# Kernel tuning notes

Hardware: AMD Instinct MI355X
Metric: run time of the kernel (lower is better)

Reference implementation:

```python
import jax, jax.numpy as jnp
import numpy as np

N_NODES = 100000
N_EDGES = 1000000
NODE_DIM = 128
EDGE_DIM = 64
IN_DIM = 2 * NODE_DIM + EDGE_DIM  # 320


def _linear_init(key, fan_in, fan_out):
    # mimic torch nn.Linear default: U(-1/sqrt(fan_in), 1/sqrt(fan_in))
    kw, kb = jax.random.split(key)
    bound = 1.0 / np.sqrt(fan_in)
    W = jax.random.uniform(kw, (fan_in, fan_out), jnp.float32, -bound, bound)
    b = jax.random.uniform(kb, (fan_out,), jnp.float32, -bound, bound)
    return W, b


def setup_inputs() -> dict:
    key = jax.random.key(0)
    ks = jax.random.split(key, 8)
    x = jax.random.normal(ks[0], (N_NODES, NODE_DIM), jnp.float32)
    edge_index = jax.random.randint(ks[1], (2, N_EDGES), 0, N_NODES, jnp.int64 if jax.config.read('jax_enable_x64') else jnp.int32)
    edge_features = jax.random.normal(ks[2], (N_EDGES, EDGE_DIM), jnp.float32)
    W1, b1 = _linear_init(ks[3], IN_DIM, 256)
    W2, b2 = _linear_init(ks[4], 256, 128)
    W3, b3 = _linear_init(ks[5], 128, 64)
    W4, b4 = _linear_init(ks[6], 64, 1)
    return {
        'x': x, 'edge_index': edge_index, 'edge_features': edge_features,
        'num_nodes': N_NODES,
        'W1': W1, 'b1': b1, 'W2': W2, 'b2': b2,
        'W3': W3, 'b3': b3, 'W4': W4, 'b4': b4,
    }


def reference(x, edge_index, edge_features, num_nodes, W1, b1, W2, b2, W3, b3, W4, b4):
    v = edge_index[0]
    u = edge_index[1]
    # gather endpoint embeddings and concat with edge features: [E, 2*node_dim+edge_dim]
    pair = jnp.concatenate([x[v], x[u], edge_features], axis=-1)
    h = jax.nn.relu(pair @ W1 + b1)
    h = jax.nn.relu(h @ W2 + b2)
    h = jax.nn.relu(h @ W3 + b3)
    pred = h @ W4 + b4  # [E, 1]
    return pred
```

## Files before the change

kernel.cpp:

```cpp
#include <hip/hip_runtime.h>
#include <hip/hip_bf16.h>

typedef __bf16 bf16;
typedef __attribute__((ext_vector_type(8))) __bf16 bf16x8;
typedef __attribute__((ext_vector_type(4))) __bf16 bf16x4;
typedef __attribute__((ext_vector_type(4))) float f32x4;

#define E_TOTAL   1000000
#define NODE_DIM  128
#define EDGE_DIM  64

#define SA_STRIDE  328
#define SH1_STRIDE 264
#define SH2_STRIDE 136

#define SMEM_BYTES 51200
#define SH2_OFF    33792

#define WS_XBF_BYTES 25600000
#define WB_W2F  163840
#define WB_W3F  (163840 + 65536)
#define WB_CANO (163840 + 65536 + 16384)
#define WB_FLAG (163840 + 65536 + 16384 + 2064)
#define WB_END  (163840 + 65536 + 16384 + 2064 + 16)
#define WS_NEED (WS_XBF_BYTES + WB_END)

__device__ inline int plausible16(const unsigned short* h) {
    int c = 0;
    for (int i = 0; i < 64; ++i) {
        int e = (h[i] >> 7) & 0xFF;
        if (e >= 90 && e <= 151) ++c;
    }
    return c;
}

__global__ void sniff(const void* x, const void* ei, const void* ef,
                      const void* W1, int* flags) {
    if (threadIdx.x == 0 && blockIdx.x == 0) {
        flags[0] = (plausible16((const unsigned short*)x)  < 52) ? 1 : 0;
        flags[1] = (plausible16((const unsigned short*)ef) < 52) ? 1 : 0;
        flags[2] = (plausible16((const unsigned short*)W1) < 52) ? 1 : 0;
        const int* w = (const int*)ei;
        int oz = 0, lo_ok = 1;
        for (int i = 1; i < 32; i += 2) if (w[i] == 0) ++oz;
        for (int i = 0; i < 32; i += 2) if ((unsigned)w[i] >= 100000u) lo_ok = 0;
        flags[3] = (oz == 16 && lo_ok) ? 1 : 0;
    }
}

__device__ inline float loadF(const void* p, int isf, int i) {
    return isf ? ((const float*)p)[i] : (float)((const bf16*)p)[i];
}

__global__ void canonicalize(const void* W1, const void* W2, const void* W3,
                             const void* b1, const void* b2, const void* b3,
                             const void* W4, const void* b4,
                             bf16* W1f, bf16* W2f, bf16* W3f,
                             float* cano, const int* flags) {
    int isf = flags[2];
    int o = blockIdx.x * 256 + threadIdx.x;
    if (o < 81920) {
        int jj = o & 7, lane = (o >> 3) & 63, t2 = o >> 9;
        int ks = t2 % 10, jt = t2 / 10;
        int k = ks * 32 + (lane >> 4) * 8 + jj;
        int n = jt * 16 + (lane & 15);
        W1f[o] = (bf16)loadF(W1, isf, k * 256 + n);
    } else if (o < 114688) {
        int o2 = o - 81920;
        int jj = o2 & 7, lane = (o2 >> 3) & 63, t2 = o2 >> 9;
        int ks = t2 & 7, jt = t2 >> 3;
        int k = ks * 32 + (lane >> 4) * 8 + jj;
        int n = jt * 16 + (lane & 15);
        W2f[o2] = (bf16)loadF(W2, isf, k * 128 + n);
    } else if (o < 122880) {
        int o3 = o - 114688;
        int jj = o3 & 7, lane = (o3 >> 3) & 63, t2 = o3 >> 9;
        int ks = t2 & 3, jt = t2 >> 2;
        int k = ks * 32 + (lane >> 4) * 8 + jj;
        int n = jt * 16 + (lane & 15);
        W3f[o3] = (bf16)loadF(W3, isf, k * 64 + n);
    } else if (o < 123396) {
        int j = o - 122880;
        float v;
        if (j < 256)       v = loadF(b1, isf, j);
        else if (j < 384)  v = loadF(b2, isf, j - 256);
        else if (j < 448)  v = loadF(b3, isf, j - 384);
        else if (j == 448) v = loadF(b4, isf, 0);
        else if (j < 452)  v = 0.f;
        else               v = loadF(W4, isf, j - 452);
        cano[j] = v;
    }
}

__global__ void convert_x(const void* x, bf16* xbf, const int* flags) {
    int i = (blockIdx.x * 256 + threadIdx.x) * 4;
    if (flags[0]) {
        const float* f = (const float*)x + i;
        bf16 v0 = (bf16)f[0], v1 = (bf16)f[1], v2 = (bf16)f[2], v3 = (bf16)f[3];
        xbf[i] = v0; xbf[i + 1] = v1; xbf[i + 2] = v2; xbf[i + 3] = v3;
    } else {
        *(unsigned long long*)(xbf + i) = *(const unsigned long long*)((const bf16*)x + i);
    }
}

__global__ __launch_bounds__(256, 3) void fused_mlp(
    const void* __restrict__ xs, const int* __restrict__ ei, const void* __restrict__ ef,
    const bf16* __restrict__ W1f, const bf16* __restrict__ W2f,
    const bf16* __restrict__ W3f,
    const float* __restrict__ cano, const int* __restrict__ flags,
    int xmode_host, float* __restrict__ out)
{
    __shared__ __align__(16) char smem[SMEM_BYTES];
    bf16* sA  = (bf16*)smem;
    bf16* sH1 = (bf16*)smem;
    bf16* sH2 = (bf16*)(smem + SH2_OFF);

    const int tid  = threadIdx.x;
    const int wave = tid >> 6;
    const int lane = tid & 63;
    const int quad = lane >> 4;
    const int l16  = lane & 15;
    const int e0   = blockIdx.x * 64;

    const int isfe = flags[1];
    const int is64 = flags[3];
    const int xm   = (xmode_host < 0) ? flags[0] : xmode_host;

    {
        const int xrow0 = tid >> 5;
        const int xseg  = tid & 31;
        const int which = xseg >> 4;
        const int xk    = (xseg & 15) << 3;
        if (xm == 0) {
            const bf16* xsb = (const bf16*)xs;
            bf16x8 xb[8];
#pragma unroll
            for (int i = 0; i < 8; ++i) {
                int row = i * 8 + xrow0;
                size_t pos = which ? (size_t)(E_TOTAL + e0 + row) : (size_t)(e0 + row);
                int node = is64 ? ei[2 * pos] : ei[pos];
                xb[i] = *(const bf16x8*)(xsb + (size_t)node * NODE_DIM + xk);
            }
#pragma unroll
            for (int i = 0; i < 8; ++i)
                *(bf16x8*)&sA[(i * 8 + xrow0) * SA_STRIDE + xseg * 8] = xb[i];
        } else {
            const float* xsf = (const float*)xs;
            float xf[8][8];
#pragma unroll
            for (int i = 0; i < 8; ++i) {
                int row = i * 8 + xrow0;
                size_t pos = which ? (size_t)(E_TOTAL + e0 + row) : (size_t)(e0 + row);
                int node = is64 ? ei[2 * pos] : ei[pos];
                const float* f = xsf + (size_t)node * NODE_DIM + xk;
#pragma unroll
                for (int j = 0; j < 8; ++j) xf[i][j] = f[j];
            }
#pragma unroll
            for (int i = 0; i < 8; ++i) {
                bf16x8 v;
#pragma unroll
                for (int j = 0; j < 8; ++j) v[j] = (bf16)xf[i][j];
                *(bf16x8*)&sA[(i * 8 + xrow0) * SA_STRIDE + xseg * 8] = v;
            }
        }
        int seg = tid & 7, r0 = tid >> 3, r1 = r0 + 32;
        int kst = 256 + seg * 8;
        if (isfe) {
            const float* f0 = (const float*)ef + (size_t)(e0 + r0) * EDGE_DIM + seg * 8;
            const float* f1 = (const float*)ef + (size_t)(e0 + r1) * EDGE_DIM + seg * 8;
            float a0[8], a1[8];
#pragma unroll
            for (int j = 0; j < 8; ++j) { a0[j] = f0[j]; a1[j] = f1[j]; }
            bf16x8 v0, v1;
#pragma unroll
            for (int j = 0; j < 8; ++j) { v0[j] = (bf16)a0[j]; v1[j] = (bf16)a1[j]; }
            *(bf16x8*)&sA[r0 * SA_STRIDE + kst] = v0;
            *(bf16x8*)&sA[r1 * SA_STRIDE + kst] = v1;
        } else {
            const bf16* eb = (const bf16*)ef;
            bf16x8 v0 = *(const bf16x8*)(eb + (size_t)(e0 + r0) * EDGE_DIM + seg * 8);
            bf16x8 v1 = *(const bf16x8*)(eb + (size_t)(e0 + r1) * EDGE_DIM + seg * 8);
            *(bf16x8*)&sA[r0 * SA_STRIDE + kst] = v0;
            *(bf16x8*)&sA[r1 * SA_STRIDE + kst] = v1;
        }
    }
    __syncthreads();

    f32x4 acc1[4][4];
#pragma unroll
    for (int p = 0; p < 4; ++p)
#pragma unroll
        for (int q = 0; q < 4; ++q)
            acc1[p][q] = (f32x4){0.f, 0.f, 0.f, 0.f};

    const bf16* w1base = W1f + (size_t)wave * (40 * 512) + lane * 8;
#pragma unroll
    for (int ks = 0; ks < 10; ++ks) {
        bf16x8 w[4], e[4];
#pragma unroll
        for (int p = 0; p < 4; ++p)
            w[p] = *(const bf16x8*)(w1base + (p * 10 + ks) * 512);
#pragma unroll
        for (int q = 0; q < 4; ++q)
            e[q] = *(const bf16x8*)&sA[(16 * q + l16) * SA_STRIDE + ks * 32 + quad * 8];
#pragma unroll
        for (int p = 0; p < 4; ++p)
#pragma unroll
            for (int q = 0; q < 4; ++q)
                acc1[p][q] = __builtin_amdgcn_mfma_f32_16x16x32_bf16(
                    w[p], e[q], acc1[p][q], 0, 0, 0);
    }
    __syncthreads();
    {
#pragma unroll
        for (int p = 0; p < 4; ++p) {
            f32x4 bias = *(const f32x4*)&cano[64 * wave + 16 * p + 4 * quad];
#pragma unroll
            for (int q = 0; q < 4; ++q) {
                bf16x4 pv;
#pragma unroll
                for (int r = 0; r < 4; ++r)
                    pv[r] = (bf16)fmaxf(acc1[p][q][r] + bias[r], 0.f);
                *(bf16x4*)&sH1[(16 * q + l16) * SH1_STRIDE + 64 * wave + 16 * p + 4 * quad] = pv;
            }
        }
    }
    __syncthreads();

    f32x4 acc2[2][4];
#pragma unroll
    for (int p = 0; p < 2; ++p)
#pragma unroll
        for (int q = 0; q < 4; ++q)
            acc2[p][q] = (f32x4){0.f, 0.f, 0.f, 0.f};
    const bf16* w2base = W2f + (size_t)wave * (16 * 512) + lane * 8;
#pragma unroll
    for (int ks = 0; ks < 8; ++ks) {
        bf16x8 w[2], e[4];
#pragma unroll
        for (int p = 0; p < 2; ++p)
            w[p] = *(const bf16x8*)(w2base + (p * 8 + ks) * 512);
#pragma unroll
        for (int q = 0; q < 4; ++q)
            e[q] = *(const bf16x8*)&sH1[(16 * q + l16) * SH1_STRIDE + ks * 32 + quad * 8];
#pragma unroll
        for (int p = 0; p < 2; ++p)
#pragma unroll
            for (int q = 0; q < 4; ++q)
                acc2[p][q] = __builtin_amdgcn_mfma_f32_16x16x32_bf16(
                    w[p], e[q], acc2[p][q], 0, 0, 0);
    }
    {
#pragma unroll
        for (int p = 0; p < 2; ++p) {
            f32x4 bias = *(const f32x4*)&cano[256 + 32 * wave + 16 * p + 4 * quad];
#pragma unroll
            for (int q = 0; q < 4; ++q) {
                bf16x4 pv;
#pragma unroll
                for (int r = 0; r < 4; ++r)
                    pv[r] = (bf16)fmaxf(acc2[p][q][r] + bias[r], 0.f);
                *(bf16x4*)&sH2[(16 * q + l16) * SH2_STRIDE + 32 * wave + 16 * p + 4 * quad] = pv;
            }
        }
    }
    __syncthreads();

    f32x4 acc3[4];
#pragma unroll
    for (int f = 0; f < 4; ++f) acc3[f] = (f32x4){0.f, 0.f, 0.f, 0.f};
    const bf16* w3base = W3f + lane * 8;
#pragma unroll
    for (int ks = 0; ks < 4; ++ks) {
        bf16x8 e = *(const bf16x8*)&sH2[(16 * wave + l16) * SH2_STRIDE + ks * 32 + quad * 8];
#pragma unroll
        for (int f = 0; f < 4; ++f) {
            bf16x8 w = *(const bf16x8*)(w3base + (f * 4 + ks) * 512);
            acc3[f] = __builtin_amdgcn_mfma_f32_16x16x32_bf16(w, e, acc3[f], 0, 0, 0);
        }
    }

    {
        float s = 0.f;
#pragma unroll
        for (int f = 0; f < 4; ++f) {
            f32x4 b3v = *(const f32x4*)&cano[384 + 16 * f + 4 * quad];
            f32x4 w4v = *(const f32x4*)&cano[452 + 16 * f + 4 * quad];
#pragma unroll
            for (int r = 0; r < 4; ++r)
                s += fmaxf(acc3[f][r] + b3v[r], 0.f) * w4v[r];
        }
        s += __shfl_xor(s, 16);
        s += __shfl_xor(s, 32);
        if (lane < 16) out[e0 + 16 * wave + l16] = s + cano[448];
    }
}

extern "C" void kernel_launch(void* const* d_in, const int* in_sizes, int n_in,
                              void* d_out, int out_size, void* d_ws, size_t ws_size,
                              hipStream_t stream) {
    const void* x  = d_in[0];
    const int*  ei = (const int*)d_in[1];
    const void* ef = d_in[2];
    const void* W1 = d_in[4];
    const void* b1 = d_in[5];
    const void* W2 = d_in[6];
    const void* b2 = d_in[7];
    const void* W3 = d_in[8];
    const void* b3 = d_in[9];
    const void* W4 = d_in[10];
    const void* b4 = d_in[11];
    float* out = (float*)d_out;

    char* ws = (char*)d_ws;
    const bool big = ws_size >= (size_t)WS_NEED;
    bf16* xbf   = (bf16*)ws;
    char* wbase = big ? (ws + WS_XBF_BYTES) : ws;
    bf16*  W1f   = (bf16*)wbase;
    bf16*  W2f   = (bf16*)(wbase + WB_W2F);
    bf16*  W3f   = (bf16*)(wbase + WB_W3F);
    float* cano  = (float*)(wbase + WB_CANO);
    int*   flags = (int*)(wbase + WB_FLAG);

    sniff<<<1, 64, 0, stream>>>(x, ei, ef, W1, flags);
    canonicalize<<<483, 256, 0, stream>>>(W1, W2, W3, b1, b2, b3, W4, b4,
                                          W1f, W2f, W3f, cano, flags);
    if (big) convert_x<<<12500, 256, 0, stream>>>(x, xbf, flags);
    fused_mlp<<<E_TOTAL / 64, 256, 0, stream>>>(
        big ? (const void*)xbf : x, ei, ef, W1f, W2f, W3f,
        cano, flags, big ? 0 : -1, out);
}
```

Baseline: 685.6 us.

## Prefetch first weight slices, raise MFMA priority, split layer-3 across waves by feature

Loads the first k-slice of W1/W2/W3 before each barrier so global latency overlaps the sync, and wraps MFMA bursts in s_setprio to favor matrix issue. Layer 3 is repartitioned so each wave computes 16 output features for all 64 edges, instead of all features for 16 edges. Partial dot products with W4 are then reduced across waves through a small shared buffer. This adds an extra barrier and 1KB of LDS, which may affect occupancy at 3 blocks per CU.

```diff
diff --git a/kernel.cpp b/kernel.cpp
--- a/kernel.cpp
+++ b/kernel.cpp
@@ -14,8 +14,9 @@
 #define SH1_STRIDE 264
 #define SH2_STRIDE 136
 
-#define SMEM_BYTES 51200
+#define SMEM_BYTES 52224
 #define SH2_OFF    33792
+#define SP_OFF     51200
 
 #define WS_XBF_BYTES 25600000
 #define WB_W2F  163840
@@ -111,9 +112,10 @@
     int xmode_host, float* __restrict__ out)
 {
     __shared__ __align__(16) char smem[SMEM_BYTES];
-    bf16* sA  = (bf16*)smem;
-    bf16* sH1 = (bf16*)smem;
-    bf16* sH2 = (bf16*)(smem + SH2_OFF);
+    bf16*  sA  = (bf16*)smem;
+    bf16*  sH1 = (bf16*)smem;
+    bf16*  sH2 = (bf16*)(smem + SH2_OFF);
+    float* sP  = (float*)(smem + SP_OFF);
 
     const int tid  = threadIdx.x;
     const int wave = tid >> 6;
@@ -125,6 +127,10 @@
     const int isfe = flags[1];
     const int is64 = flags[3];
     const int xm   = (xmode_host < 0) ? flags[0] : xmode_host;
+
+    const bf16* w1base = W1f + (size_t)wave * (40 * 512) + lane * 8;
+    const bf16* w2base = W2f + (size_t)wave * (16 * 512) + lane * 8;
+    const bf16* w3base = W3f + (size_t)wave * (4 * 512) + lane * 8;
 
     {
         const int xrow0 = tid >> 5;
@@ -185,6 +191,10 @@
             *(bf16x8*)&sA[r1 * SA_STRIDE + kst] = v1;
         }
     }
+    bf16x8 w1pre[4];
+#pragma unroll
+    for (int p = 0; p < 4; ++p)
+        w1pre[p] = *(const bf16x8*)(w1base + (p * 10 + 0) * 512);
     __syncthreads();
 
     f32x4 acc1[4][4];
@@ -194,22 +204,24 @@
         for (int q = 0; q < 4; ++q)
             acc1[p][q] = (f32x4){0.f, 0.f, 0.f, 0.f};
 
-    const bf16* w1base = W1f + (size_t)wave * (40 * 512) + lane * 8;
 #pragma unroll
     for (int ks = 0; ks < 10; ++ks) {
         bf16x8 w[4], e[4];
 #pragma unroll
         for (int p = 0; p < 4; ++p)
-            w[p] = *(const bf16x8*)(w1base + (p * 10 + ks) * 512);
+            w[p] = (ks == 0) ? w1pre[p]
+                             : *(const bf16x8*)(w1base + (p * 10 + ks) * 512);
 #pragma unroll
         for (int q = 0; q < 4; ++q)
             e[q] = *(const bf16x8*)&sA[(16 * q + l16) * SA_STRIDE + ks * 32 + quad * 8];
+        __builtin_amdgcn_s_setprio(1);
 #pragma unroll
         for (int p = 0; p < 4; ++p)
 #pragma unroll
             for (int q = 0; q < 4; ++q)
                 acc1[p][q] = __builtin_amdgcn_mfma_f32_16x16x32_bf16(
                     w[p], e[q], acc1[p][q], 0, 0, 0);
+        __builtin_amdgcn_s_setprio(0);
     }
     __syncthreads();
     {
@@ -226,6 +238,10 @@
             }
         }
     }
+    bf16x8 w2pre[2];
+#pragma unroll
+    for (int p = 0; p < 2; ++p)
+        w2pre[p] = *(const bf16x8*)(w2base + (p * 8 + 0) * 512);
     __syncthreads();
 
     f32x4 acc2[2][4];
@@ -234,22 +250,24 @@
 #pragma unroll
         for (int q = 0; q < 4; ++q)
             acc2[p][q] = (f32x4){0.f, 0.f, 0.f, 0.f};
-    const bf16* w2base = W2f + (size_t)wave * (16 * 512) + lane * 8;
 #pragma unroll
     for (int ks = 0; ks < 8; ++ks) {
         bf16x8 w[2], e[4];
 #pragma unroll
         for (int p = 0; p < 2; ++p)
-            w[p] = *(const bf16x8*)(w2base + (p * 8 + ks) * 512);
+            w[p] = (ks == 0) ? w2pre[p]
+                             : *(const bf16x8*)(w2base + (p * 8 + ks) * 512);
 #pragma unroll
         for (int q = 0; q < 4; ++q)
             e[q] = *(const bf16x8*)&sH1[(16 * q + l16) * SH1_STRIDE + ks * 32 + quad * 8];
+        __builtin_amdgcn_s_setprio(1);
 #pragma unroll
         for (int p = 0; p < 2; ++p)
 #pragma unroll
             for (int q = 0; q < 4; ++q)
                 acc2[p][q] = __builtin_amdgcn_mfma_f32_16x16x32_bf16(
                     w[p], e[q], acc2[p][q], 0, 0, 0);
+        __builtin_amdgcn_s_setprio(0);
     }
     {
 #pragma unroll
@@ -265,35 +283,49 @@
             }
         }
     }
+    bf16x8 w3pre = *(const bf16x8*)(w3base + 0 * 512);
     __syncthreads();
 
     f32x4 acc3[4];
 #pragma unroll
-    for (int f = 0; f < 4; ++f) acc3[f] = (f32x4){0.f, 0.f, 0.f, 0.f};
-    const bf16* w3base = W3f + lane * 8;
+    for (int q = 0; q < 4; ++q) acc3[q] = (f32x4){0.f, 0.f, 0.f, 0.f};
 #pragma unroll
     for (int ks = 0; ks < 4; ++ks) {
-        bf16x8 e = *(const bf16x8*)&sH2[(16 * wave + l16) * SH2_STRIDE + ks * 32 + quad * 8];
-#pragma unroll
-        for (int f = 0; f < 4; ++f) {
-            bf16x8 w = *(const bf16x8*)(w3base + (f * 4 + ks) * 512);
-            acc3[f] = __builtin_amdgcn_mfma_f32_16x16x32_bf16(w, e, acc3[f], 0, 0, 0);
-        }
+        bf16x8 w = (ks == 0) ? w3pre : *(const bf16x8*)(w3base + ks * 512);
+        bf16x8 e[4];
+#pragma unroll
+        for (int q = 0; q < 4; ++q)
+            e[q] = *(const bf16x8*)&sH2[(16 * q + l16) * SH2_STRIDE + ks * 32 + quad * 8];
+        __builtin_amdgcn_s_setprio(1);
+#pragma unroll
+        for (int q = 0; q < 4; ++q)
+            acc3[q] = __builtin_amdgcn_mfma_f32_16x16x32_bf16(w, e[q], acc3[q], 0, 0, 0);
+        __builtin_amdgcn_s_setprio(0);
     }
 
     {
-        float s = 0.f;
-#pragma unroll
-        for (int f = 0; f < 4; ++f) {
-            f32x4 b3v = *(const f32x4*)&cano[384 + 16 * f + 4 * quad];
-            f32x4 w4v = *(const f32x4*)&cano[452 + 16 * f + 4 * quad];
+        f32x4 b3v = *(const f32x4*)&cano[384 + 16 * wave + 4 * quad];
+        f32x4 w4v = *(const f32x4*)&cano[452 + 16 * wave + 4 * quad];
+        float pq[4];
+#pragma unroll
+        for (int q = 0; q < 4; ++q) {
+            float s = 0.f;
 #pragma unroll
             for (int r = 0; r < 4; ++r)
-                s += fmaxf(acc3[f][r] + b3v[r], 0.f) * w4v[r];
-        }
-        s += __shfl_xor(s, 16);
-        s += __shfl_xor(s, 32);
-        if (lane < 16) out[e0 + 16 * wave + l16] = s + cano[448];
+                s += fmaxf(acc3[q][r] + b3v[r], 0.f) * w4v[r];
+            s += __shfl_xor(s, 16);
+            s += __shfl_xor(s, 32);
+            pq[q] = s;
+        }
+        float mine = (quad == 0) ? pq[0] : (quad == 1) ? pq[1]
+                   : (quad == 2) ? pq[2] : pq[3];
+        sP[(16 * quad + l16) * 4 + wave] = mine;
+    }
+    __syncthreads();
+
+    if (tid < 64) {
+        f32x4 v = *(const f32x4*)&sP[tid * 4];
+        out[e0 + tid] = v[0] + v[1] + v[2] + v[3] + cano[448];
     }
 }
 
```

Result: faster. 612.5 us (-10.7%).
